# Kernel tuning notes

Measured on AMD Instinct MI355X. Metric: run time of the kernel, lower is better.

The kernel has to match this reference:

```python
import jax, jax.numpy as jnp
import numpy as np

C = 16  # CHANNELS


def _dwconv3x3(x, k2d):
    # x: [N, C, H, W]; k2d: [3,3] replicated per channel (depthwise, groups=C)
    k = jnp.broadcast_to(k2d, (C, 1, 3, 3)).astype(x.dtype)
    return jax.lax.conv_general_dilated(
        x, k, window_strides=(1, 1), padding=[(1, 1), (1, 1)],
        feature_group_count=C, dimension_numbers=("NCHW", "OIHW", "NCHW"))


def setup_inputs() -> dict:
    key = jax.random.key(0)
    k0, k1, k2, k3, k4, k5 = jax.random.split(key, 6)
    H = W = 1024
    return {
        "input": jax.random.uniform(k0, (1, C, H, W), dtype=jnp.float32),
        "stoch": jax.random.uniform(k1, (1, 1, H, W), dtype=jnp.float32),
        "w1": jax.random.normal(k2, (128, C * 3), dtype=jnp.float32) * 0.05,
        "b1": jax.random.normal(k3, (128,), dtype=jnp.float32) * 0.02,
        "w2": jax.random.normal(k4, (16, 128), dtype=jnp.float32) * 0.05,
        "b2": jax.random.normal(k5, (16,), dtype=jnp.float32) * 0.02,
    }


def reference(input, stoch, w1, b1, w2, b2):
    _, _, H, W = input.shape
    fy = jnp.array([[1.0, 2.0, 1.0], [0.0, 0.0, 0.0], [-1.0, -2.0, -1.0]], dtype=input.dtype)
    fx = fy.T
    fid = jnp.array([[0.0, 0.0, 0.0], [0.0, 1.0, 0.0], [0.0, 0.0, 0.0]], dtype=input.dtype)

    # depthwise convs, clamped and detached (stop_gradient mirrors .detach())
    sx = jax.lax.stop_gradient(jnp.clip(_dwconv3x3(input, fx), 0.0, 1.0))
    idc = jax.lax.stop_gradient(jnp.clip(_dwconv3x3(input, fid), 0.0, 1.0))
    # NOTE: original computes sy but uses [sx, sx, id] in perception

    perception = jnp.concatenate([sx, sx, idc], axis=1)          # [1, 3C, H, W]
    perception = jnp.transpose(perception, (0, 2, 3, 1)).reshape(H * W, C * 3)

    h = jax.nn.relu(perception @ w1.T + b1)                       # [HW, 128]
    x = h @ w2.T + b2                                             # [HW, 16]
    diff = jnp.transpose(x.reshape(1, H, W, C), (0, 3, 1, 2))     # [1, C, H, W]

    mask = (stoch < 0.5).astype(input.dtype)                      # [1,1,H,W]
    diff = diff * mask

    alive_in = input[:, 3, :, :]                                  # [1, H, W]
    pooled = jax.lax.reduce_window(
        alive_in, -jnp.inf, jax.lax.max, (1, 3, 3), (1, 1, 1),
        [(0, 0), (1, 1), (1, 1)])
    alive = (pooled > 0.1).astype(input.dtype)                    # [1,H,W] -> broadcasts over C

    updated = jnp.clip((diff + idc) * alive, 0.0, 1.0)
    return updated
```

## Files before the change

kernel.cpp:

```cpp
#include <hip/hip_runtime.h>

#define HH 1024
#define WW 1024
#define NPIX (HH * WW)

typedef __bf16 bf8 __attribute__((ext_vector_type(8)));
typedef float  f4  __attribute__((ext_vector_type(4)));

static __device__ __forceinline__ float bf2f(unsigned short s) {
    unsigned u = ((unsigned)s) << 16;
    return __builtin_bit_cast(float, u);
}
static __device__ __forceinline__ unsigned short f2bf(float f) {
    unsigned u = __builtin_bit_cast(unsigned, f);
    u += 0x7fffu + ((u >> 16) & 1u);
    return (unsigned short)(u >> 16);
}
static __device__ __forceinline__ unsigned packbf2(float a, float b) {
    return (unsigned)f2bf(a) | ((unsigned)f2bf(b) << 16);
}

__global__ __launch_bounds__(256) void ca_mfma_kernel(
    const float* __restrict__ input,
    const float* __restrict__ stoch,
    const float* __restrict__ w1,
    const float* __restrict__ b1,
    const float* __restrict__ w2,
    const float* __restrict__ b2,
    float* __restrict__ out)
{
    __shared__ __align__(16) unsigned short s_P[256 * 40];
    __shared__ __align__(16) unsigned short s_W1[128 * 40];
    __shared__ __align__(16) unsigned short s_W2[16 * 128];
    __shared__ __align__(16) unsigned short s_H[4 * 2048];
    __shared__ float s_mask[256];
    __shared__ float s_alive[256];

    const int t = threadIdx.x;

    for (int i = t; i < 128 * 16; i += 256) {
        int j = i >> 4, k = (i & 15) * 2;
        const float* row = w1 + j * 48;
        float v0, v1;
        if (k < 16) { v0 = row[k] + row[k + 16];  v1 = row[k + 1] + row[k + 17]; }
        else        { v0 = row[k + 16];           v1 = row[k + 17]; }
        *reinterpret_cast<unsigned*>(&s_W1[j * 40 + k]) = packbf2(v0, v1);
    }
    for (int i = t; i < 16 * 64; i += 256) {
        int c = i >> 6, j = (i & 63) * 2;
        *reinterpret_cast<unsigned*>(&s_W2[c * 128 + j]) = packbf2(w2[c * 128 + j], w2[c * 128 + j + 1]);
    }

    const int pix = blockIdx.x * 256 + t;
    const int y = pix >> 10;
    const int x = pix & (WW - 1);
    const bool xl = (x > 0), xr = (x < WW - 1);
    const bool yu = (y > 0), yd = (y < HH - 1);

    float sx[16], idc[16];
    #pragma unroll
    for (int c = 0; c < 16; ++c) {
        const float* ip = input + c * NPIX + pix;
        float center = ip[0];
        float a  = (xl && yu) ? ip[-WW - 1] : 0.f;
        float bb = (xr && yu) ? ip[-WW + 1] : 0.f;
        float cl = xl ? ip[-1] : 0.f;
        float cr = xr ? ip[+1] : 0.f;
        float dl = (xl && yd) ? ip[WW - 1] : 0.f;
        float dr = (xr && yd) ? ip[WW + 1] : 0.f;
        float s = (a - bb) + 2.f * (cl - cr) + (dl - dr);
        sx[c]  = fminf(fmaxf(s, 0.f), 1.f);
        idc[c] = fminf(fmaxf(center, 0.f), 1.f);
    }
    {
        const float* ip = input + 3 * NPIX + pix;
        float m = ip[0];
        if (xl) m = fmaxf(m, ip[-1]);
        if (xr) m = fmaxf(m, ip[+1]);
        if (yu) {
            m = fmaxf(m, ip[-WW]);
            if (xl) m = fmaxf(m, ip[-WW - 1]);
            if (xr) m = fmaxf(m, ip[-WW + 1]);
        }
        if (yd) {
            m = fmaxf(m, ip[WW]);
            if (xl) m = fmaxf(m, ip[WW - 1]);
            if (xr) m = fmaxf(m, ip[WW + 1]);
        }
        s_alive[t] = (m > 0.1f) ? 1.f : 0.f;
    }
    s_mask[t] = (stoch[pix] < 0.5f) ? 1.f : 0.f;

    {
        unsigned prow[16];
        #pragma unroll
        for (int q = 0; q < 8; ++q) prow[q]     = packbf2(sx[2 * q],  sx[2 * q + 1]);
        #pragma unroll
        for (int q = 0; q < 8; ++q) prow[8 + q] = packbf2(idc[2 * q], idc[2 * q + 1]);
        #pragma unroll
        for (int qq = 0; qq < 4; ++qq)
            *reinterpret_cast<uint4*>(&s_P[t * 40 + qq * 8]) =
                make_uint4(prow[4*qq], prow[4*qq+1], prow[4*qq+2], prow[4*qq+3]);
    }

    __syncthreads();

    const int w  = t >> 6;
    const int l  = t & 63;
    const int p  = l & 15;
    const int g  = l >> 4;
    const int swz = (p & 7) << 4;

    bf8 af1[8];
    #pragma unroll
    for (int t8 = 0; t8 < 8; ++t8)
        af1[t8] = *reinterpret_cast<const bf8*>(&s_W1[(16 * t8 + p) * 40 + g * 8]);
    bf8 af2[4];
    #pragma unroll
    for (int kt = 0; kt < 4; ++kt)
        af2[kt] = *reinterpret_cast<const bf8*>(&s_W2[p * 128 + kt * 32 + g * 8]);
    f4 b1f[8];
    #pragma unroll
    for (int t8 = 0; t8 < 8; ++t8)
        b1f[t8] = *reinterpret_cast<const f4*>(b1 + 16 * t8 + 4 * g);
    f4 b2f = *reinterpret_cast<const f4*>(b2 + 4 * g);

    unsigned short* sHw = &s_H[w * 2048];

    for (int u = 0; u < 4; ++u) {
        const int rowP = w * 64 + u * 16 + p;
        bf8 bP = *reinterpret_cast<const bf8*>(&s_P[rowP * 40 + g * 8]);

        f4 acc1[8];
        #pragma unroll
        for (int t8 = 0; t8 < 8; ++t8)
            acc1[t8] = __builtin_amdgcn_mfma_f32_16x16x32_bf16(af1[t8], bP, b1f[t8], 0, 0, 0);

        #pragma unroll
        for (int t8 = 0; t8 < 8; ++t8) {
            float h0 = fmaxf(acc1[t8][0], 0.f), h1 = fmaxf(acc1[t8][1], 0.f);
            float h2 = fmaxf(acc1[t8][2], 0.f), h3 = fmaxf(acc1[t8][3], 0.f);
            unsigned u0 = packbf2(h0, h1), u1 = packbf2(h2, h3);
            int off = (p * 256 + 32 * t8 + 8 * g) ^ swz;
            *reinterpret_cast<uint2*>(reinterpret_cast<char*>(sHw) + off) = make_uint2(u0, u1);
        }
        __syncthreads();

        f4 acc2 = b2f;
        #pragma unroll
        for (int kt = 0; kt < 4; ++kt) {
            int off = (p * 256 + 64 * kt + 16 * g) ^ swz;
            bf8 bH = *reinterpret_cast<const bf8*>(reinterpret_cast<char*>(sHw) + off);
            acc2 = __builtin_amdgcn_mfma_f32_16x16x32_bf16(af2[kt], bH, acc2, 0, 0, 0);
        }

        float mk = s_mask[rowP];
        float al = s_alive[rowP];
        uint2 idcu = *reinterpret_cast<const uint2*>(
            reinterpret_cast<const char*>(s_P) + rowP * 80 + 32 + 8 * g);
        float id0 = bf2f((unsigned short)(idcu.x & 0xffff));
        float id1 = bf2f((unsigned short)(idcu.x >> 16));
        float id2 = bf2f((unsigned short)(idcu.y & 0xffff));
        float id3 = bf2f((unsigned short)(idcu.y >> 16));

        const int pixg = blockIdx.x * 256 + rowP;
        float v0 = fminf(fmaxf((acc2[0] * mk + id0) * al, 0.f), 1.f);
        float v1 = fminf(fmaxf((acc2[1] * mk + id1) * al, 0.f), 1.f);
        float v2 = fminf(fmaxf((acc2[2] * mk + id2) * al, 0.f), 1.f);
        float v3 = fminf(fmaxf((acc2[3] * mk + id3) * al, 0.f), 1.f);
        out[(4 * g + 0) * NPIX + pixg] = v0;
        out[(4 * g + 1) * NPIX + pixg] = v1;
        out[(4 * g + 2) * NPIX + pixg] = v2;
        out[(4 * g + 3) * NPIX + pixg] = v3;

        __syncthreads();
    }
}

extern "C" void kernel_launch(void* const* d_in, const int* in_sizes, int n_in,
                              void* d_out, int out_size, void* d_ws, size_t ws_size,
                              hipStream_t stream) {
    const float* input = (const float*)d_in[0];
    const float* stoch = (const float*)d_in[1];
    const float* w1    = (const float*)d_in[2];
    const float* b1    = (const float*)d_in[3];
    const float* w2    = (const float*)d_in[4];
    const float* b2    = (const float*)d_in[5];
    float* out = (float*)d_out;

    dim3 grid(NPIX / 256);
    dim3 block(256);
    hipLaunchKernelGGL(ca_mfma_kernel, grid, block, 0, stream,
                       input, stoch, w1, b1, w2, b2, out);
}
```

Baseline: 198.6 us.

## Feed first-MFMA outputs directly into second MFMA via register permutation

Permutes the W1 row order and the bias indexing so that each lane's first-layer MFMA accumulator outputs line up with the B-operand layout of the second-layer MFMA. The hidden activations can then be packed to bf16 in registers, which removes the s_H shared-memory staging buffer, its swizzled writes and reads, and two block-wide barriers per iteration. It also sets launch_bounds min-blocks to 4 and fully unrolls the u loop, which may raise register pressure in exchange for higher occupancy and less LDS use.

```diff
diff --git a/kernel.cpp b/kernel.cpp
--- a/kernel.cpp
+++ b/kernel.cpp
@@ -6,6 +6,7 @@
 
 typedef __bf16 bf8 __attribute__((ext_vector_type(8)));
 typedef float  f4  __attribute__((ext_vector_type(4)));
+typedef unsigned uv4 __attribute__((ext_vector_type(4)));
 
 static __device__ __forceinline__ float bf2f(unsigned short s) {
     unsigned u = ((unsigned)s) << 16;
@@ -20,7 +21,7 @@
     return (unsigned)f2bf(a) | ((unsigned)f2bf(b) << 16);
 }
 
-__global__ __launch_bounds__(256) void ca_mfma_kernel(
+__global__ __launch_bounds__(256, 4) void ca_mfma_kernel(
     const float* __restrict__ input,
     const float* __restrict__ stoch,
     const float* __restrict__ w1,
@@ -32,7 +33,6 @@
     __shared__ __align__(16) unsigned short s_P[256 * 40];
     __shared__ __align__(16) unsigned short s_W1[128 * 40];
     __shared__ __align__(16) unsigned short s_W2[16 * 128];
-    __shared__ __align__(16) unsigned short s_H[4 * 2048];
     __shared__ float s_mask[256];
     __shared__ float s_alive[256];
 
@@ -44,7 +44,9 @@
         float v0, v1;
         if (k < 16) { v0 = row[k] + row[k + 16];  v1 = row[k + 1] + row[k + 17]; }
         else        { v0 = row[k + 16];           v1 = row[k + 17]; }
-        *reinterpret_cast<unsigned*>(&s_W1[j * 40 + k]) = packbf2(v0, v1);
+        int t8 = ((j >> 5) & 3) | (((j >> 2) & 1) << 2);
+        int m  = (((j >> 3) & 3) << 2) | (j & 3);
+        *reinterpret_cast<unsigned*>(&s_W1[(t8 * 16 + m) * 40 + k]) = packbf2(v0, v1);
     }
     for (int i = t; i < 16 * 64; i += 256) {
         int c = i >> 6, j = (i & 63) * 2;
@@ -109,7 +111,6 @@
     const int l  = t & 63;
     const int p  = l & 15;
     const int g  = l >> 4;
-    const int swz = (p & 7) << 4;
 
     bf8 af1[8];
     #pragma unroll
@@ -122,35 +123,25 @@
     f4 b1f[8];
     #pragma unroll
     for (int t8 = 0; t8 < 8; ++t8)
-        b1f[t8] = *reinterpret_cast<const f4*>(b1 + 16 * t8 + 4 * g);
+        b1f[t8] = *reinterpret_cast<const f4*>(b1 + 32 * (t8 & 3) + 8 * g + 4 * (t8 >> 2));
     f4 b2f = *reinterpret_cast<const f4*>(b2 + 4 * g);
 
-    unsigned short* sHw = &s_H[w * 2048];
-
+    #pragma unroll
     for (int u = 0; u < 4; ++u) {
         const int rowP = w * 64 + u * 16 + p;
         bf8 bP = *reinterpret_cast<const bf8*>(&s_P[rowP * 40 + g * 8]);
 
-        f4 acc1[8];
-        #pragma unroll
-        for (int t8 = 0; t8 < 8; ++t8)
-            acc1[t8] = __builtin_amdgcn_mfma_f32_16x16x32_bf16(af1[t8], bP, b1f[t8], 0, 0, 0);
-
-        #pragma unroll
-        for (int t8 = 0; t8 < 8; ++t8) {
-            float h0 = fmaxf(acc1[t8][0], 0.f), h1 = fmaxf(acc1[t8][1], 0.f);
-            float h2 = fmaxf(acc1[t8][2], 0.f), h3 = fmaxf(acc1[t8][3], 0.f);
-            unsigned u0 = packbf2(h0, h1), u1 = packbf2(h2, h3);
-            int off = (p * 256 + 32 * t8 + 8 * g) ^ swz;
-            *reinterpret_cast<uint2*>(reinterpret_cast<char*>(sHw) + off) = make_uint2(u0, u1);
-        }
-        __syncthreads();
-
         f4 acc2 = b2f;
         #pragma unroll
         for (int kt = 0; kt < 4; ++kt) {
-            int off = (p * 256 + 64 * kt + 16 * g) ^ swz;
-            bf8 bH = *reinterpret_cast<const bf8*>(reinterpret_cast<char*>(sHw) + off);
+            f4 h0 = __builtin_amdgcn_mfma_f32_16x16x32_bf16(af1[kt],     bP, b1f[kt],     0, 0, 0);
+            f4 h1 = __builtin_amdgcn_mfma_f32_16x16x32_bf16(af1[kt + 4], bP, b1f[kt + 4], 0, 0, 0);
+            unsigned q0 = packbf2(fmaxf(h0[0], 0.f), fmaxf(h0[1], 0.f));
+            unsigned q1 = packbf2(fmaxf(h0[2], 0.f), fmaxf(h0[3], 0.f));
+            unsigned q2 = packbf2(fmaxf(h1[0], 0.f), fmaxf(h1[1], 0.f));
+            unsigned q3 = packbf2(fmaxf(h1[2], 0.f), fmaxf(h1[3], 0.f));
+            uv4 bv = {q0, q1, q2, q3};
+            bf8 bH = __builtin_bit_cast(bf8, bv);
             acc2 = __builtin_amdgcn_mfma_f32_16x16x32_bf16(af2[kt], bH, acc2, 0, 0, 0);
         }
 
@@ -172,8 +163,6 @@
         out[(4 * g + 1) * NPIX + pixg] = v1;
         out[(4 * g + 2) * NPIX + pixg] = v2;
         out[(4 * g + 3) * NPIX + pixg] = v3;
-
-        __syncthreads();
     }
 }
 
```

New measurement: 181.9 us. 1.09x faster.
